# Performance work log

Measured on AMD Instinct MI355X. Metric: run time of the kernel, lower is better.

## Reference

```python
import jax, jax.numpy as jnp
import numpy as np

B, T, H, L, O = 128, 1024, 512, 2, 1
SCALE = 0.02  # keep tanh/sigmoid in sane range


def setup_inputs() -> dict:
    key = jax.random.key(0)
    ks = jax.random.split(key, 13)
    return {
        "input": jax.random.normal(ks[0], (B, 8), jnp.float32),
        "hidden": jax.random.normal(ks[1], (L, B, H), jnp.float32) * 0.5,
        "encoder_outputs": jax.random.normal(ks[2], (B, T, H), jnp.float32),
        "attn_w": jax.random.normal(ks[3], (1, (L + 1) * H), jnp.float32) * SCALE,
        "attn_b": jnp.zeros((1,), jnp.float32),
        "comb_w": jax.random.normal(ks[4], (H, H + O), jnp.float32) * SCALE,
        "comb_b": jnp.zeros((H,), jnp.float32),
        "gru_w_ih": jax.random.normal(ks[5], (L, 3 * H, H), jnp.float32) * SCALE,
        "gru_w_hh": jax.random.normal(ks[6], (L, 3 * H, H), jnp.float32) * SCALE,
        "gru_b_ih": jnp.zeros((L, 3 * H), jnp.float32),
        "gru_b_hh": jnp.zeros((L, 3 * H), jnp.float32),
        "out_w": jax.random.normal(ks[7], (O, H), jnp.float32) * SCALE,
        "out_b": jnp.zeros((O,), jnp.float32),
    }


def reference(input, hidden, encoder_outputs, attn_w, attn_b, comb_w, comb_b,
              gru_w_ih, gru_w_hh, gru_b_ih, gru_b_hh, out_w, out_b):
    # input0 = input[:, -1].unsqueeze(1) -> [B, 1]
    input0 = input[:, -1:]
    # hidden [L,B,H] -> hidden_attn [B, L*H]
    hidden_attn = jnp.transpose(hidden, (1, 0, 2)).reshape(hidden.shape[1], -1)
    # Vectorized additive-attention scores (original loops over T):
    # score[b,t] = [hidden_attn_b ; enc_bt] @ attn_w.T + attn_b
    w = attn_w[0]                      # [(L+1)*H]
    w_h, w_e = w[: L * H], w[L * H:]   # [L*H], [H]
    score = (hidden_attn @ w_h)[:, None] + jnp.einsum('bth,h->bt', encoder_outputs, w_e) + attn_b[0]
    attn_weights = jax.nn.softmax(score, axis=1)          # [B, T]
    attn_applied = jnp.einsum('bt,bth->bh', attn_weights, encoder_outputs)  # [B, H]
    # attn_combine + relu (dropout_p = 0 -> identity)
    comb_in = jnp.concatenate([input0, attn_applied], axis=1)  # [B, 1+H]
    x = jax.nn.relu(comb_in @ comb_w.T + comb_b)               # [B, H]
    # single-step multi-layer GRU (PyTorch gate order: r, z, n)
    new_hidden = []
    for l in range(L):
        gx = x @ gru_w_ih[l].T + gru_b_ih[l]             # [B, 3H]
        gh = hidden[l] @ gru_w_hh[l].T + gru_b_hh[l]     # [B, 3H]
        xr, xz, xn = jnp.split(gx, 3, axis=1)
        hr, hz, hn = jnp.split(gh, 3, axis=1)
        r = jax.nn.sigmoid(xr + hr)
        z = jax.nn.sigmoid(xz + hz)
        n = jnp.tanh(xn + r * hn)
        h_new = (1.0 - z) * n + z * hidden[l]
        new_hidden.append(h_new)
        x = h_new
    hidden_out = jnp.stack(new_hidden, axis=0)           # [L, B, H]
    output = x @ out_w.T + out_b                         # [B, O]
    return output, hidden_out, attn_weights[:, None, :]
```

## Files before the change

### kernel.cpp

```cpp
#include <hip/hip_runtime.h>
#include <math.h>

#define B 128
#define T 1024
#define H 512
#define L 2
#define G3H 1536
#define C 8
#define TC 128
#define TT 16
#define KS 4

__global__ __launch_bounds__(256, 4)
void attn_fused_kernel(const float* __restrict__ enc,
                       const float* __restrict__ attn_w,
                       float* __restrict__ score_out,
                       float* __restrict__ part,
                       float* __restrict__ stats) {
    int c = blockIdx.x, b = blockIdx.y;
    int tid = threadIdx.x, lane = tid & 63, wave = tid >> 6;
    __shared__ float tile[TT * H];
    __shared__ float s_tile[TT];

    float we[8];
#pragma unroll
    for (int j = 0; j < 8; j++) we[j] = attn_w[L * H + lane + j * 64];

    float m_run = -1e30f, l_run = 0.0f;
    float accx = 0.0f, accy = 0.0f;
    const float* encb = enc + ((size_t)b * T + c * TC) * H;

    for (int t0 = 0; t0 < TC; t0 += TT) {
        __syncthreads();
#pragma unroll
        for (int k = 0; k < 8; k++) {
            *(float4*)(tile + 4 * tid + k * 1024) =
                *(const float4*)(encb + (size_t)t0 * H + 4 * tid + k * 1024);
        }
        __syncthreads();
#pragma unroll
        for (int r = 0; r < 4; r++) {
            int row = wave * 4 + r;
            const float* tr = tile + row * H;
            float d = 0.0f;
#pragma unroll
            for (int j = 0; j < 8; j++) d += we[j] * tr[lane + j * 64];
#pragma unroll
            for (int off = 32; off; off >>= 1) d += __shfl_xor(d, off);
            if (lane == 0) {
                s_tile[row] = d;
                score_out[b * T + c * TC + t0 + row] = d;
            }
        }
        __syncthreads();
        float s[TT], tmax = -1e30f;
#pragma unroll
        for (int i = 0; i < TT; i++) { s[i] = s_tile[i]; tmax = fmaxf(tmax, s[i]); }
        float m_new = fmaxf(m_run, tmax);
        float alpha = __expf(m_run - m_new);
        accx *= alpha; accy *= alpha;
        float wsum = 0.0f;
#pragma unroll
        for (int i = 0; i < TT; i++) {
            float w = __expf(s[i] - m_new);
            wsum += w;
            accx += w * tile[i * H + tid];
            accy += w * tile[i * H + tid + 256];
        }
        l_run = l_run * alpha + wsum;
        m_run = m_new;
    }
    part[((size_t)c * B + b) * H + tid]       = accx;
    part[((size_t)c * B + b) * H + tid + 256] = accy;
    if (tid == 0) {
        stats[(c * B + b) * 2]     = m_run;
        stats[(c * B + b) * 2 + 1] = l_run;
    }
}

__global__ void attn_reduce_kernel(const float* __restrict__ part,
                                   const float* __restrict__ stats,
                                   const float* __restrict__ score,
                                   float* __restrict__ attn_applied,
                                   float* __restrict__ attnw) {
    int b = blockIdx.x, tid = threadIdx.x;
    float mc[C], lc[C], m_fin = -1e30f;
#pragma unroll
    for (int k = 0; k < C; k++) {
        mc[k] = stats[(k * B + b) * 2];
        lc[k] = stats[(k * B + b) * 2 + 1];
        m_fin = fmaxf(m_fin, mc[k]);
    }
    float l_fin = 0.0f;
#pragma unroll
    for (int k = 0; k < C; k++) l_fin += lc[k] * __expf(mc[k] - m_fin);
    float inv = 1.0f / l_fin;
    float ax = 0.0f, ay = 0.0f;
#pragma unroll
    for (int k = 0; k < C; k++) {
        float sc = __expf(mc[k] - m_fin);
        ax += sc * part[((size_t)k * B + b) * H + tid];
        ay += sc * part[((size_t)k * B + b) * H + tid + 256];
    }
    attn_applied[(size_t)b * H + tid]       = ax * inv;
    attn_applied[(size_t)b * H + tid + 256] = ay * inv;
    float4 sv = *(const float4*)(score + b * T + tid * 4);
    float4 ov = { __expf(sv.x - m_fin) * inv, __expf(sv.y - m_fin) * inv,
                  __expf(sv.z - m_fin) * inv, __expf(sv.w - m_fin) * inv };
    *(float4*)(attnw + b * T + tid * 4) = ov;
}

__global__ void comb_kernel(const float* __restrict__ attn_applied,
                            const float* __restrict__ input,
                            const float* __restrict__ comb_w,
                            const float* __restrict__ comb_b,
                            float* __restrict__ x_out) {
    int q = blockIdx.x, b = blockIdx.y, tid = threadIdx.x;
    int lane = tid & 63, wave = tid >> 6;
    float in0 = input[b * 8 + 7];
    float areg[8];
#pragma unroll
    for (int j = 0; j < 8; j++) areg[j] = attn_applied[(size_t)b * H + j * 64 + lane];
    for (int r = 0; r < 32; r++) {
        int h = q * 128 + wave * 32 + r;
        const float* wr = comb_w + (size_t)h * (H + 1);
        float d = 0.0f;
#pragma unroll
        for (int j = 0; j < 8; j++) d += areg[j] * wr[1 + j * 64 + lane];
#pragma unroll
        for (int off = 32; off; off >>= 1) d += __shfl_xor(d, off);
        if (lane == 0)
            x_out[(size_t)b * H + h] = fmaxf(0.0f, d + in0 * wr[0] + comb_b[h]);
    }
}

__global__ void gemm_kernel(const float* __restrict__ A0,
                            const float* __restrict__ A1,
                            const float* __restrict__ W0,
                            const float* __restrict__ W1,
                            float* __restrict__ C0,
                            float* __restrict__ C1) {
    int z = blockIdx.z;
    int sel = z & 1, ks = z >> 1;
    const float* A = sel ? A1 : A0;
    const float* W = sel ? W1 : W0;
    float* Cp = (sel ? C1 : C0) + (size_t)ks * B * G3H;
    __shared__ float As[32][33];
    __shared__ float Ws[32][33];
    int n0 = blockIdx.x * 32, m0 = blockIdx.y * 32;
    int tid = threadIdx.x;
    int lrow = tid >> 3;
    int lcol = (tid & 7) * 4;
    int tm = (tid >> 4) * 2;
    int tn = (tid & 15) * 2;
    float a00 = 0, a01 = 0, a10 = 0, a11 = 0;
    int kbeg = ks * (H / KS), kend = kbeg + H / KS;
    for (int k0 = kbeg; k0 < kend; k0 += 32) {
        float4 av = *(const float4*)(A + (size_t)(m0 + lrow) * H + k0 + lcol);
        float4 wv = *(const float4*)(W + (size_t)(n0 + lrow) * H + k0 + lcol);
        __syncthreads();
        As[lrow][lcol] = av.x; As[lrow][lcol + 1] = av.y;
        As[lrow][lcol + 2] = av.z; As[lrow][lcol + 3] = av.w;
        Ws[lrow][lcol] = wv.x; Ws[lrow][lcol + 1] = wv.y;
        Ws[lrow][lcol + 2] = wv.z; Ws[lrow][lcol + 3] = wv.w;
        __syncthreads();
#pragma unroll
        for (int k = 0; k < 32; k++) {
            float x0 = As[tm][k], x1 = As[tm + 1][k];
            float w0 = Ws[tn][k], w1 = Ws[tn + 1][k];
            a00 += x0 * w0; a01 += x0 * w1;
            a10 += x1 * w0; a11 += x1 * w1;
        }
    }
    Cp[(size_t)(m0 + tm) * G3H + n0 + tn]         = a00;
    Cp[(size_t)(m0 + tm) * G3H + n0 + tn + 1]     = a01;
    Cp[(size_t)(m0 + tm + 1) * G3H + n0 + tn]     = a10;
    Cp[(size_t)(m0 + tm + 1) * G3H + n0 + tn + 1] = a11;
}

__global__ void gates_kernel(const float* __restrict__ gx,
                             const float* __restrict__ gh,
                             const float* __restrict__ b_ih,
                             const float* __restrict__ b_hh,
                             const float* __restrict__ hprev,
                             float* __restrict__ hid_out,
                             float* __restrict__ x_out) {
    int idx = blockIdx.x * 256 + threadIdx.x;
    int b = idx >> 9, h = idx & 511;
    size_t gb = (size_t)b * G3H;
    float xr = b_ih[h], xz = b_ih[H + h], xn = b_ih[2 * H + h];
    float hr = b_hh[h], hz = b_hh[H + h], hn = b_hh[2 * H + h];
#pragma unroll
    for (int k = 0; k < KS; k++) {
        size_t o = (size_t)k * B * G3H + gb;
        xr += gx[o + h];         xz += gx[o + H + h];     xn += gx[o + 2 * H + h];
        hr += gh[o + h];         hz += gh[o + H + h];     hn += gh[o + 2 * H + h];
    }
    float hp = hprev[(size_t)b * H + h];
    float r = 1.0f / (1.0f + expf(-(xr + hr)));
    float z = 1.0f / (1.0f + expf(-(xz + hz)));
    float n = tanhf(xn + r * hn);
    float hnew = (1.0f - z) * n + z * hp;
    hid_out[(size_t)b * H + h] = hnew;
    x_out[(size_t)b * H + h] = hnew;
}

__global__ void out_kernel(const float* __restrict__ x,
                           const float* __restrict__ out_w,
                           const float* __restrict__ out_b,
                           float* __restrict__ out) {
    int b = blockIdx.x, lane = threadIdx.x;
    const float4 w0 = *(const float4*)(out_w + lane * 8);
    const float4 w1 = *(const float4*)(out_w + lane * 8 + 4);
    const float4 x0 = *(const float4*)(x + (size_t)b * H + lane * 8);
    const float4 x1 = *(const float4*)(x + (size_t)b * H + lane * 8 + 4);
    float d = x0.x * w0.x + x0.y * w0.y + x0.z * w0.z + x0.w * w0.w
            + x1.x * w1.x + x1.y * w1.y + x1.z * w1.z + x1.w * w1.w;
#pragma unroll
    for (int off = 32; off; off >>= 1) d += __shfl_xor(d, off);
    if (lane == 0) out[b] = d + out_b[0];
}

extern "C" void kernel_launch(void* const* d_in, const int* in_sizes, int n_in,
                              void* d_out, int out_size, void* d_ws, size_t ws_size,
                              hipStream_t stream) {
    const float* input  = (const float*)d_in[0];
    const float* hidden = (const float*)d_in[1];
    const float* enc    = (const float*)d_in[2];
    const float* attn_w = (const float*)d_in[3];
    const float* comb_w = (const float*)d_in[5];
    const float* comb_b = (const float*)d_in[6];
    const float* w_ih   = (const float*)d_in[7];
    const float* w_hh   = (const float*)d_in[8];
    const float* b_ih   = (const float*)d_in[9];
    const float* b_hh   = (const float*)d_in[10];
    const float* out_w  = (const float*)d_in[11];
    const float* out_b  = (const float*)d_in[12];

    float* out = (float*)d_out;
    float* hid_out = out + B;
    float* attnw   = out + B + L * B * H;

    float* ws      = (float*)d_ws;
    float* score   = ws;
    float* part    = score + B * T;
    float* stats   = part + C * B * H;
    float* attnapp = stats + C * B * 2;
    float* x       = attnapp + B * H;
    float* gx      = x + B * H;
    float* gh      = gx + KS * B * G3H;

    attn_fused_kernel<<<dim3(C, B), 256, 0, stream>>>(enc, attn_w, score, part, stats);
    attn_reduce_kernel<<<dim3(B), 256, 0, stream>>>(part, stats, score, attnapp, attnw);
    comb_kernel<<<dim3(4, B), 256, 0, stream>>>(attnapp, input, comb_w, comb_b, x);

    for (int l = 0; l < L; l++) {
        const float* hl = hidden + (size_t)l * B * H;
        gemm_kernel<<<dim3(G3H / 32, B / 32, 2 * KS), 256, 0, stream>>>(
            x, hl,
            w_ih + (size_t)l * G3H * H, w_hh + (size_t)l * G3H * H,
            gx, gh);
        gates_kernel<<<dim3(B * H / 256), 256, 0, stream>>>(
            gx, gh, b_ih + l * G3H, b_hh + l * G3H, hl,
            hid_out + (size_t)l * B * H, x);
    }
    out_kernel<<<dim3(B), 64, 0, stream>>>(x, out_w, out_b, out);
}
```

Measured before the change: 458.5 us.

## Double-buffer encoder tiles with async global-to-LDS loads in attention kernel

The attention kernel now loads encoder tiles straight from global memory into LDS with global_load_lds and double-buffers them, so the fetch of the next tile overlaps the score and softmax-accumulate work on the current one. The tile is halved to 8 rows to fit two buffers in LDS, and one of the per-tile barriers is replaced by an explicit LDS waitcnt plus s_barrier. The score dot product now reads each lane's contiguous 8 floats as vectors. The risks are more loop iterations and barriers per chunk, and correctness that depends on the implicit barrier fences waiting for the async loads.

```diff
diff --git a/kernel.cpp b/kernel.cpp
--- a/kernel.cpp
+++ b/kernel.cpp
@@ -8,8 +8,12 @@
 #define G3H 1536
 #define C 8
 #define TC 128
-#define TT 16
+#define TT 8
+#define NT (TC / TT)
 #define KS 4
+
+#define GLOBAL_AS __attribute__((address_space(1)))
+#define LDS_AS    __attribute__((address_space(3)))
 
 __global__ __launch_bounds__(256, 4)
 void attn_fused_kernel(const float* __restrict__ enc,
@@ -19,53 +23,71 @@
                        float* __restrict__ stats) {
     int c = blockIdx.x, b = blockIdx.y;
     int tid = threadIdx.x, lane = tid & 63, wave = tid >> 6;
-    __shared__ float tile[TT * H];
+    __shared__ float tile[2][TT * H];
     __shared__ float s_tile[TT];
 
-    float we[8];
-#pragma unroll
-    for (int j = 0; j < 8; j++) we[j] = attn_w[L * H + lane + j * 64];
+    const float4 we0 = *(const float4*)(attn_w + L * H + lane * 8);
+    const float4 we1 = *(const float4*)(attn_w + L * H + lane * 8 + 4);
+
+    const float* encb = enc + ((size_t)b * T + c * TC) * H;
+    const GLOBAL_AS float* gsrc = (const GLOBAL_AS float*)encb;
+    LDS_AS float* ldst = (LDS_AS float*)(&tile[0][0]);
+
+#define STAGE(buf, t0)                                                        \
+    {                                                                         \
+        const GLOBAL_AS float* g = gsrc + (size_t)(t0) * H;                   \
+        LDS_AS float* lb = ldst + (buf) * (TT * H);                           \
+        _Pragma("unroll")                                                     \
+        for (int k = 0; k < 4; k++) {                                         \
+            __builtin_amdgcn_global_load_lds(                                 \
+                (const GLOBAL_AS void*)(g + k * 1024 + tid * 4),              \
+                (LDS_AS void*)(lb + k * 1024 + tid * 4), 16, 0, 0);           \
+        }                                                                     \
+    }
 
     float m_run = -1e30f, l_run = 0.0f;
     float accx = 0.0f, accy = 0.0f;
-    const float* encb = enc + ((size_t)b * T + c * TC) * H;
-
-    for (int t0 = 0; t0 < TC; t0 += TT) {
+
+    STAGE(0, 0);
+    for (int t = 0; t < NT; t++) {
         __syncthreads();
-#pragma unroll
-        for (int k = 0; k < 8; k++) {
-            *(float4*)(tile + 4 * tid + k * 1024) =
-                *(const float4*)(encb + (size_t)t0 * H + 4 * tid + k * 1024);
-        }
-        __syncthreads();
-#pragma unroll
-        for (int r = 0; r < 4; r++) {
-            int row = wave * 4 + r;
-            const float* tr = tile + row * H;
-            float d = 0.0f;
-#pragma unroll
-            for (int j = 0; j < 8; j++) d += we[j] * tr[lane + j * 64];
+        if (t + 1 < NT) STAGE((t + 1) & 1, (t + 1) * TT);
+        const float* tb = &tile[t & 1][0];
+
+#pragma unroll
+        for (int r = 0; r < 2; r++) {
+            int row = wave * 2 + r;
+            const float* tr = tb + row * H + lane * 8;
+            float4 e0 = *(const float4*)(tr);
+            float4 e1 = *(const float4*)(tr + 4);
+            float d = e0.x * we0.x + e0.y * we0.y + e0.z * we0.z + e0.w * we0.w
+                    + e1.x * we1.x + e1.y * we1.y + e1.z * we1.z + e1.w * we1.w;
 #pragma unroll
             for (int off = 32; off; off >>= 1) d += __shfl_xor(d, off);
             if (lane == 0) {
                 s_tile[row] = d;
-                score_out[b * T + c * TC + t0 + row] = d;
+                score_out[b * T + c * TC + t * TT + row] = d;
             }
         }
-        __syncthreads();
-        float s[TT], tmax = -1e30f;
-#pragma unroll
-        for (int i = 0; i < TT; i++) { s[i] = s_tile[i]; tmax = fmaxf(tmax, s[i]); }
+        __builtin_amdgcn_s_waitcnt(0xC07F);
+        __builtin_amdgcn_s_barrier();
+
+        float sarr[TT], tmax = -1e30f;
+#pragma unroll
+        for (int i = 0; i < TT; i++) {
+            sarr[i] = s_tile[i];
+            tmax = fmaxf(tmax, sarr[i]);
+        }
         float m_new = fmaxf(m_run, tmax);
         float alpha = __expf(m_run - m_new);
         accx *= alpha; accy *= alpha;
         float wsum = 0.0f;
 #pragma unroll
         for (int i = 0; i < TT; i++) {
-            float w = __expf(s[i] - m_new);
+            float w = __expf(sarr[i] - m_new);
             wsum += w;
-            accx += w * tile[i * H + tid];
-            accy += w * tile[i * H + tid + 256];
+            accx += w * tb[i * H + tid];
+            accy += w * tb[i * H + tid + 256];
         }
         l_run = l_run * alpha + wsum;
         m_run = m_new;
@@ -76,6 +98,7 @@
         stats[(c * B + b) * 2]     = m_run;
         stats[(c * B + b) * 2 + 1] = l_run;
     }
+#undef STAGE
 }
 
 __global__ void attn_reduce_kernel(const float* __restrict__ part,
```

Result: no change. 459.5 us (+0.2%).
